# Performance work log

Hardware: AMD Instinct MI355X
Metric: run time of the kernel (lower is better)

## Reference

```python
import jax, jax.numpy as jnp
import numpy as np

EPS = 1e-10
COMMITMENT_COST = 0.25


def setup_inputs() -> dict:
    key = jax.random.key(0)
    k1, k2, k3, k4 = jax.random.split(key, 4)
    return {
        "x": jax.random.normal(k1, (32, 64, 64, 64), dtype=jnp.float32),  # NCHW, C=D=64
        "emb0": jax.random.normal(k2, (512, 64), dtype=jnp.float32),
        "emb1": jax.random.normal(k3, (512, 64), dtype=jnp.float32),
        "emb2": jax.random.normal(k4, (512, 64), dtype=jnp.float32),
        "idx": 1,
    }


def reference(x, emb0, emb1, emb2, idx):
    # NCHW -> NHWC, flatten to [N, D]
    inputs = jnp.transpose(x, (0, 2, 3, 1))
    in_shape = inputs.shape
    D = in_shape[-1]
    flat = inputs.reshape(-1, D)  # [N, D]

    if idx == 0:
        codes = emb0
    elif idx == 1:
        codes = jnp.concatenate([emb0, emb1], axis=0)
    else:
        codes = jnp.concatenate([emb0, emb2], axis=0)  # [K, D]

    distances = (
        jnp.sum(flat * flat, axis=1, keepdims=True)
        + jnp.sum(codes * codes, axis=1)
        - 2.0 * jnp.matmul(flat, codes.T)
    )
    enc_idx = jnp.argmin(distances, axis=1)  # [N]

    # one-hot @ codes is just a gather
    quantized = codes[enc_idx].reshape(in_shape)

    e_latent_loss = jnp.mean((jax.lax.stop_gradient(quantized) - inputs) ** 2)
    q_latent_loss = jnp.mean((quantized - jax.lax.stop_gradient(inputs)) ** 2)
    loss = q_latent_loss + COMMITMENT_COST * e_latent_loss

    # straight-through estimator
    quantized_st = inputs + jax.lax.stop_gradient(quantized - inputs)

    K = codes.shape[0]
    N = flat.shape[0]
    avg_probs = jnp.zeros((K,), dtype=flat.dtype).at[enc_idx].add(1.0) / N
    perplexity = jnp.exp(-jnp.sum(avg_probs * jnp.log(avg_probs + EPS)))

    return jnp.transpose(quantized_st, (0, 3, 1, 2)), loss, perplexity
```

## Files before the change

### kernel.cpp

```cpp
#include <hip/hip_runtime.h>
#include <math.h>

#define NROWS   131072
#define DFEAT   64
#define KHALF   512
#define HW      4096
#define CHW     262144
#define NQOUT   8388608

typedef __attribute__((ext_vector_type(8))) short   bf16x8;
typedef __attribute__((ext_vector_type(4))) float   f32x4;

__device__ __forceinline__ unsigned short f2bf(float f) {
    unsigned int u = __float_as_uint(f);
    u += 0x7FFFu + ((u >> 16) & 1u);
    return (unsigned short)(u >> 16);
}
__device__ __forceinline__ float bf2f(unsigned short h) {
    return __uint_as_float(((unsigned int)h) << 16);
}

__global__ void vq_cnorm(const float* __restrict__ e0, const float* __restrict__ e1,
                         const float* __restrict__ e2, const int* __restrict__ idxp,
                         float* __restrict__ cnh) {
    int k = blockIdx.x * blockDim.x + threadIdx.x;
    if (k >= 1024) return;
    int idx = idxp[0];
    const float* sel = (idx == 2) ? e2 : e1;
    const float* row = (k < KHALF) ? (e0 + (size_t)k * DFEAT)
                                   : (sel + (size_t)(k - KHALF) * DFEAT);
    float s = 0.f;
#pragma unroll
    for (int c = 0; c < DFEAT; ++c) s = fmaf(row[c], row[c], s);
    cnh[k] = 0.5f * s;
}

__global__ void vq_pack(const float* __restrict__ e0, const float* __restrict__ e1,
                        const float* __restrict__ e2, const int* __restrict__ idxp,
                        unsigned short* __restrict__ fragbuf) {
    int tau = blockIdx.x * 256 + threadIdx.x;
    int tile = tau >> 8;
    int rem  = tau & 255;
    int f    = rem >> 6;
    int L    = rem & 63;
    int code = tile * 16 + (L & 15);
    int kb   = (f & 1) * 32 + (L >> 4) * 8;
    int lo_f = f >> 1;
    int idx  = idxp[0];
    const float* sel = (idx == 2) ? e2 : e1;
    const float* src = (code < KHALF) ? (e0 + (size_t)code * DFEAT)
                                      : (sel + (size_t)(code - KHALF) * DFEAT);
    unsigned short* dst = fragbuf + (size_t)tau * 8;
#pragma unroll
    for (int j = 0; j < 8; ++j) {
        float v = src[kb + j];
        unsigned short hb = f2bf(v);
        dst[j] = lo_f ? f2bf(v - bf2f(hb)) : hb;
    }
}

__global__ __launch_bounds__(256, 2) void vq_main(
        const float* __restrict__ x,
        const float* __restrict__ e0, const float* __restrict__ e1,
        const float* __restrict__ e2, const int* __restrict__ idxp,
        const float* __restrict__ cnh, const unsigned short* __restrict__ fragbuf,
        float* __restrict__ out, float* __restrict__ loss_acc,
        int* __restrict__ hist) {
    __shared__ float xsq_s[256];
    __shared__ float sc_s[256];
    __shared__ int   bk_s[256];

    const int t = threadIdx.x;
    const int w = t >> 6;
    const int L = t & 63;
    const int q = L >> 4;
    const int m = L & 15;

    const int rowbase = blockIdx.x * 256;
    const int n  = rowbase >> 12;
    const int s0 = rowbase & 4095;

    const int idx = idxp[0];
    const float* sel = (idx == 2) ? e2 : e1;
    const int ntiles = (idx == 0) ? 32 : 64;

    bf16x8 ahi[4][2], alo[4][2];
    const float* xb = x + (size_t)n * CHW + (s0 + w * 64);
#pragma unroll
    for (int rt = 0; rt < 4; ++rt) {
        const float* xr = xb + rt * 16 + m;
        float xs = 0.f;
#pragma unroll
        for (int h = 0; h < 2; ++h) {
#pragma unroll
            for (int j = 0; j < 8; ++j) {
                int c = h * 32 + q * 8 + j;
                float v = xr[(size_t)c * HW];
                xs = fmaf(v, v, xs);
                unsigned short hb = f2bf(v);
                unsigned short lb = f2bf(v - bf2f(hb));
                ahi[rt][h][j] = (short)hb;
                alo[rt][h][j] = (short)lb;
            }
        }
        xs += __shfl_xor(xs, 16, 64);
        xs += __shfl_xor(xs, 32, 64);
        if (q == 0) xsq_s[w * 64 + rt * 16 + m] = xs;
    }

    const bf16x8* fb = (const bf16x8*)fragbuf;
    float best[16];
    int   bidx[16];
#pragma unroll
    for (int i = 0; i < 16; ++i) { best[i] = -3.4e38f; bidx[i] = 0; }

    bf16x8 bc0 = fb[0 * 64 + L];
    bf16x8 bc1 = fb[1 * 64 + L];
    bf16x8 bc2 = fb[2 * 64 + L];
    bf16x8 bc3 = fb[3 * 64 + L];
    float  cnc = cnh[m];

    for (int tt = 0; tt < ntiles; ++tt) {
        const int tn = (tt + 1 < ntiles) ? tt + 1 : tt;
        bf16x8 bn0 = fb[(tn * 4 + 0) * 64 + L];
        bf16x8 bn1 = fb[(tn * 4 + 1) * 64 + L];
        bf16x8 bn2 = fb[(tn * 4 + 2) * 64 + L];
        bf16x8 bn3 = fb[(tn * 4 + 3) * 64 + L];
        float  cnn = cnh[tn * 16 + m];
        const int kt = tt * 16 + m;
#pragma unroll
        for (int rt = 0; rt < 4; ++rt) {
            f32x4 acc = {0.f, 0.f, 0.f, 0.f};
            acc = __builtin_amdgcn_mfma_f32_16x16x32_bf16(ahi[rt][0], bc0, acc, 0, 0, 0);
            acc = __builtin_amdgcn_mfma_f32_16x16x32_bf16(ahi[rt][1], bc1, acc, 0, 0, 0);
            acc = __builtin_amdgcn_mfma_f32_16x16x32_bf16(ahi[rt][0], bc2, acc, 0, 0, 0);
            acc = __builtin_amdgcn_mfma_f32_16x16x32_bf16(ahi[rt][1], bc3, acc, 0, 0, 0);
            acc = __builtin_amdgcn_mfma_f32_16x16x32_bf16(alo[rt][0], bc0, acc, 0, 0, 0);
            acc = __builtin_amdgcn_mfma_f32_16x16x32_bf16(alo[rt][1], bc1, acc, 0, 0, 0);
            acc = __builtin_amdgcn_mfma_f32_16x16x32_bf16(alo[rt][0], bc2, acc, 0, 0, 0);
            acc = __builtin_amdgcn_mfma_f32_16x16x32_bf16(alo[rt][1], bc3, acc, 0, 0, 0);
#pragma unroll
            for (int r = 0; r < 4; ++r) {
                float s = acc[r] - cnc;
                if (s > best[rt * 4 + r]) { best[rt * 4 + r] = s; bidx[rt * 4 + r] = kt; }
            }
        }
        bc0 = bn0; bc1 = bn1; bc2 = bn2; bc3 = bn3; cnc = cnn;
    }

#pragma unroll
    for (int i = 0; i < 16; ++i) {
        float b = best[i]; int k = bidx[i];
#pragma unroll
        for (int off = 1; off < 16; off <<= 1) {
            float ob = __shfl_xor(b, off, 64);
            int   ok = __shfl_xor(k, off, 64);
            if (ob > b || (ob == b && ok < k)) { b = ob; k = ok; }
        }
        if (m == 0) {
            int row = w * 64 + (i >> 2) * 16 + q * 4 + (i & 3);
            sc_s[row] = b; bk_s[row] = k;
        }
    }
    __syncthreads();

    const int k   = bk_s[t];
    float dist    = xsq_s[t] - 2.f * sc_s[t];
    float l = dist;
#pragma unroll
    for (int off = 32; off > 0; off >>= 1) l += __shfl_down(l, off, 64);
    if (L == 0) atomicAdd(loss_acc, l);
    atomicAdd(&hist[k], 1);

    const float* cp = (k < KHALF) ? (e0 + (size_t)k * DFEAT)
                                  : (sel + (size_t)(k - KHALF) * DFEAT);
    const float4* cp4 = (const float4*)cp;
    float* op = out + (size_t)n * CHW + (s0 + t);
#pragma unroll
    for (int c4 = 0; c4 < 16; ++c4) {
        float4 v = cp4[c4];
        op[(size_t)(4 * c4 + 0) * HW] = v.x;
        op[(size_t)(4 * c4 + 1) * HW] = v.y;
        op[(size_t)(4 * c4 + 2) * HW] = v.z;
        op[(size_t)(4 * c4 + 3) * HW] = v.w;
    }
}

__global__ void vq_finalize(const float* __restrict__ wsf, const int* __restrict__ hist,
                            float* __restrict__ out) {
    __shared__ double partial[16];
    const int t = threadIdx.x;
    double p = (double)hist[t] / (double)NROWS;
    double term = p * log(p + 1e-10);
#pragma unroll
    for (int off = 32; off > 0; off >>= 1) term += __shfl_down(term, off, 64);
    if ((t & 63) == 0) partial[t >> 6] = term;
    __syncthreads();
    if (t == 0) {
        double s = 0.0;
        for (int i = 0; i < 16; ++i) s += partial[i];
        out[NQOUT + 1] = (float)exp(-s);
        out[NQOUT]     = 1.25f * (wsf[0] / (float)NQOUT);
    }
}

extern "C" void kernel_launch(void* const* d_in, const int* in_sizes, int n_in,
                              void* d_out, int out_size, void* d_ws, size_t ws_size,
                              hipStream_t stream) {
    const float* x  = (const float*)d_in[0];
    const float* e0 = (const float*)d_in[1];
    const float* e1 = (const float*)d_in[2];
    const float* e2 = (const float*)d_in[3];
    const int* idxp = (const int*)d_in[4];
    float* out = (float*)d_out;

    float* wsf      = (float*)d_ws;
    float* loss_acc = wsf;
    int*   hist     = (int*)(wsf + 256);
    float* cnh      = wsf + 2048;
    unsigned short* fragbuf = (unsigned short*)(wsf + 4096);

    hipMemsetAsync(d_ws, 0, 1280 * sizeof(float), stream);
    vq_cnorm<<<4, 256, 0, stream>>>(e0, e1, e2, idxp, cnh);
    vq_pack<<<64, 256, 0, stream>>>(e0, e1, e2, idxp, fragbuf);
    vq_main<<<NROWS / 256, 256, 0, stream>>>(x, e0, e1, e2, idxp, cnh, fragbuf,
                                             out, loss_acc, hist);
    vq_finalize<<<1, 1024, 0, stream>>>(wsf, hist, out);
}
```

Before: 193.8 us.

## Fuse prep kernels, halve rows per block, and finalize in last block

Merges the memset, codebook-norm and fragment-pack kernels into one prep kernel, and folds the perplexity/loss finalize into the main kernel using a last-block-done atomic counter. Each main block now handles 128 rows instead of 256, which doubles the grid to 1024 blocks, raises the launch-bounds occupancy target to 4, and splits the output scatter across all 256 threads. The aim is to cut launch overhead and improve latency hiding. The trade-off is that each codebook fragment load is reused over fewer rows, so fragment traffic per row doubles, and the threadfence plus completion counter add some serialization.

```diff
diff --git a/kernel.cpp b/kernel.cpp
--- a/kernel.cpp
+++ b/kernel.cpp
@@ -7,6 +7,7 @@
 #define HW      4096
 #define CHW     262144
 #define NQOUT   8388608
+#define NBLK    1024
 
 typedef __attribute__((ext_vector_type(8))) short   bf16x8;
 typedef __attribute__((ext_vector_type(4))) float   f32x4;
@@ -20,25 +21,25 @@
     return __uint_as_float(((unsigned int)h) << 16);
 }
 
-__global__ void vq_cnorm(const float* __restrict__ e0, const float* __restrict__ e1,
-                         const float* __restrict__ e2, const int* __restrict__ idxp,
-                         float* __restrict__ cnh) {
-    int k = blockIdx.x * blockDim.x + threadIdx.x;
-    if (k >= 1024) return;
+__global__ void vq_prep(const float* __restrict__ e0, const float* __restrict__ e1,
+                        const float* __restrict__ e2, const int* __restrict__ idxp,
+                        float* __restrict__ wsf, float* __restrict__ cnh,
+                        unsigned short* __restrict__ fragbuf) {
+    int tau = blockIdx.x * 256 + threadIdx.x;
+    if (tau < 1536) wsf[tau] = 0.f;
+
     int idx = idxp[0];
     const float* sel = (idx == 2) ? e2 : e1;
-    const float* row = (k < KHALF) ? (e0 + (size_t)k * DFEAT)
-                                   : (sel + (size_t)(k - KHALF) * DFEAT);
-    float s = 0.f;
-#pragma unroll
-    for (int c = 0; c < DFEAT; ++c) s = fmaf(row[c], row[c], s);
-    cnh[k] = 0.5f * s;
-}
-
-__global__ void vq_pack(const float* __restrict__ e0, const float* __restrict__ e1,
-                        const float* __restrict__ e2, const int* __restrict__ idxp,
-                        unsigned short* __restrict__ fragbuf) {
-    int tau = blockIdx.x * 256 + threadIdx.x;
+
+    if (tau < 1024) {
+        const float* row = (tau < KHALF) ? (e0 + (size_t)tau * DFEAT)
+                                         : (sel + (size_t)(tau - KHALF) * DFEAT);
+        float s = 0.f;
+#pragma unroll
+        for (int c = 0; c < DFEAT; ++c) s = fmaf(row[c], row[c], s);
+        cnh[tau] = 0.5f * s;
+    }
+
     int tile = tau >> 8;
     int rem  = tau & 255;
     int f    = rem >> 6;
@@ -46,8 +47,6 @@
     int code = tile * 16 + (L & 15);
     int kb   = (f & 1) * 32 + (L >> 4) * 8;
     int lo_f = f >> 1;
-    int idx  = idxp[0];
-    const float* sel = (idx == 2) ? e2 : e1;
     const float* src = (code < KHALF) ? (e0 + (size_t)code * DFEAT)
                                       : (sel + (size_t)(code - KHALF) * DFEAT);
     unsigned short* dst = fragbuf + (size_t)tau * 8;
@@ -59,16 +58,18 @@
     }
 }
 
-__global__ __launch_bounds__(256, 2) void vq_main(
+__global__ __launch_bounds__(256, 4) void vq_main(
         const float* __restrict__ x,
         const float* __restrict__ e0, const float* __restrict__ e1,
         const float* __restrict__ e2, const int* __restrict__ idxp,
         const float* __restrict__ cnh, const unsigned short* __restrict__ fragbuf,
         float* __restrict__ out, float* __restrict__ loss_acc,
-        int* __restrict__ hist) {
-    __shared__ float xsq_s[256];
-    __shared__ float sc_s[256];
-    __shared__ int   bk_s[256];
+        int* __restrict__ hist, int* __restrict__ done_ctr) {
+    __shared__ float  xsq_s[128];
+    __shared__ float  sc_s[128];
+    __shared__ int    bk_s[128];
+    __shared__ int    islast_s;
+    __shared__ double pp_s[4];
 
     const int t = threadIdx.x;
     const int w = t >> 6;
@@ -76,7 +77,7 @@
     const int q = L >> 4;
     const int m = L & 15;
 
-    const int rowbase = blockIdx.x * 256;
+    const int rowbase = blockIdx.x * 128;
     const int n  = rowbase >> 12;
     const int s0 = rowbase & 4095;
 
@@ -84,10 +85,10 @@
     const float* sel = (idx == 2) ? e2 : e1;
     const int ntiles = (idx == 0) ? 32 : 64;
 
-    bf16x8 ahi[4][2], alo[4][2];
-    const float* xb = x + (size_t)n * CHW + (s0 + w * 64);
-#pragma unroll
-    for (int rt = 0; rt < 4; ++rt) {
+    bf16x8 ahi[2][2], alo[2][2];
+    const float* xb = x + (size_t)n * CHW + (s0 + w * 32);
+#pragma unroll
+    for (int rt = 0; rt < 2; ++rt) {
         const float* xr = xb + rt * 16 + m;
         float xs = 0.f;
 #pragma unroll
@@ -105,14 +106,14 @@
         }
         xs += __shfl_xor(xs, 16, 64);
         xs += __shfl_xor(xs, 32, 64);
-        if (q == 0) xsq_s[w * 64 + rt * 16 + m] = xs;
+        if (q == 0) xsq_s[w * 32 + rt * 16 + m] = xs;
     }
 
     const bf16x8* fb = (const bf16x8*)fragbuf;
-    float best[16];
-    int   bidx[16];
-#pragma unroll
-    for (int i = 0; i < 16; ++i) { best[i] = -3.4e38f; bidx[i] = 0; }
+    float best[8];
+    int   bidx[8];
+#pragma unroll
+    for (int i = 0; i < 8; ++i) { best[i] = -3.4e38f; bidx[i] = 0; }
 
     bf16x8 bc0 = fb[0 * 64 + L];
     bf16x8 bc1 = fb[1 * 64 + L];
@@ -120,6 +121,7 @@
     bf16x8 bc3 = fb[3 * 64 + L];
     float  cnc = cnh[m];
 
+#pragma unroll 2
     for (int tt = 0; tt < ntiles; ++tt) {
         const int tn = (tt + 1 < ntiles) ? tt + 1 : tt;
         bf16x8 bn0 = fb[(tn * 4 + 0) * 64 + L];
@@ -129,7 +131,7 @@
         float  cnn = cnh[tn * 16 + m];
         const int kt = tt * 16 + m;
 #pragma unroll
-        for (int rt = 0; rt < 4; ++rt) {
+        for (int rt = 0; rt < 2; ++rt) {
             f32x4 acc = {0.f, 0.f, 0.f, 0.f};
             acc = __builtin_amdgcn_mfma_f32_16x16x32_bf16(ahi[rt][0], bc0, acc, 0, 0, 0);
             acc = __builtin_amdgcn_mfma_f32_16x16x32_bf16(ahi[rt][1], bc1, acc, 0, 0, 0);
@@ -149,7 +151,7 @@
     }
 
 #pragma unroll
-    for (int i = 0; i < 16; ++i) {
+    for (int i = 0; i < 8; ++i) {
         float b = best[i]; int k = bidx[i];
 #pragma unroll
         for (int off = 1; off < 16; off <<= 1) {
@@ -158,49 +160,69 @@
             if (ob > b || (ob == b && ok < k)) { b = ob; k = ok; }
         }
         if (m == 0) {
-            int row = w * 64 + (i >> 2) * 16 + q * 4 + (i & 3);
+            int row = w * 32 + (i >> 2) * 16 + q * 4 + (i & 3);
             sc_s[row] = b; bk_s[row] = k;
         }
     }
     __syncthreads();
 
-    const int k   = bk_s[t];
-    float dist    = xsq_s[t] - 2.f * sc_s[t];
-    float l = dist;
-#pragma unroll
-    for (int off = 32; off > 0; off >>= 1) l += __shfl_down(l, off, 64);
-    if (L == 0) atomicAdd(loss_acc, l);
-    atomicAdd(&hist[k], 1);
-
-    const float* cp = (k < KHALF) ? (e0 + (size_t)k * DFEAT)
-                                  : (sel + (size_t)(k - KHALF) * DFEAT);
-    const float4* cp4 = (const float4*)cp;
-    float* op = out + (size_t)n * CHW + (s0 + t);
-#pragma unroll
-    for (int c4 = 0; c4 < 16; ++c4) {
-        float4 v = cp4[c4];
-        op[(size_t)(4 * c4 + 0) * HW] = v.x;
-        op[(size_t)(4 * c4 + 1) * HW] = v.y;
-        op[(size_t)(4 * c4 + 2) * HW] = v.z;
-        op[(size_t)(4 * c4 + 3) * HW] = v.w;
-    }
-}
-
-__global__ void vq_finalize(const float* __restrict__ wsf, const int* __restrict__ hist,
-                            float* __restrict__ out) {
-    __shared__ double partial[16];
-    const int t = threadIdx.x;
-    double p = (double)hist[t] / (double)NROWS;
-    double term = p * log(p + 1e-10);
-#pragma unroll
-    for (int off = 32; off > 0; off >>= 1) term += __shfl_down(term, off, 64);
-    if ((t & 63) == 0) partial[t >> 6] = term;
+    if (t < 128) {
+        const int k = bk_s[t];
+        float dist = xsq_s[t] - 2.f * sc_s[t];
+        float l = dist;
+#pragma unroll
+        for (int off = 32; off > 0; off >>= 1) l += __shfl_down(l, off, 64);
+        if (L == 0) atomicAdd(loss_acc, l);
+        atomicAdd(&hist[k], 1);
+    }
+
+    {
+        const int row  = t & 127;
+        const int half = t >> 7;
+        const int k = bk_s[row];
+        const float* cp = ((k < KHALF) ? (e0 + (size_t)k * DFEAT)
+                                       : (sel + (size_t)(k - KHALF) * DFEAT)) + half * 32;
+        const float4* cp4 = (const float4*)cp;
+        float* op = out + (size_t)n * CHW + (s0 + row);
+#pragma unroll
+        for (int c4 = 0; c4 < 8; ++c4) {
+            float4 v = cp4[c4];
+            int c = half * 32 + 4 * c4;
+            op[(size_t)(c + 0) * HW] = v.x;
+            op[(size_t)(c + 1) * HW] = v.y;
+            op[(size_t)(c + 2) * HW] = v.z;
+            op[(size_t)(c + 3) * HW] = v.w;
+        }
+    }
+
+    __threadfence();
     __syncthreads();
     if (t == 0) {
-        double s = 0.0;
-        for (int i = 0; i < 16; ++i) s += partial[i];
-        out[NQOUT + 1] = (float)exp(-s);
-        out[NQOUT]     = 1.25f * (wsf[0] / (float)NQOUT);
+        int tk = __hip_atomic_fetch_add(done_ctr, 1, __ATOMIC_ACQ_REL,
+                                        __HIP_MEMORY_SCOPE_AGENT);
+        islast_s = (tk == NBLK - 1);
+    }
+    __syncthreads();
+    if (islast_s) {
+        double term = 0.0;
+#pragma unroll
+        for (int j = 0; j < 4; ++j) {
+            int c = __hip_atomic_load(&hist[t * 4 + j], __ATOMIC_RELAXED,
+                                      __HIP_MEMORY_SCOPE_AGENT);
+            double p = (double)c / (double)NROWS;
+            term += p * log(p + 1e-10);
+        }
+#pragma unroll
+        for (int off = 32; off > 0; off >>= 1) term += __shfl_down(term, off, 64);
+        if (L == 0) pp_s[w] = term;
+        __syncthreads();
+        if (t == 0) {
+            double s = pp_s[0] + pp_s[1] + pp_s[2] + pp_s[3];
+            float lacc = __hip_atomic_load(loss_acc, __ATOMIC_RELAXED,
+                                           __HIP_MEMORY_SCOPE_AGENT);
+            out[NQOUT + 1] = (float)exp(-s);
+            out[NQOUT]     = 1.25f * (lacc / (float)NQOUT);
+        }
     }
 }
 
@@ -217,13 +239,11 @@
     float* wsf      = (float*)d_ws;
     float* loss_acc = wsf;
     int*   hist     = (int*)(wsf + 256);
+    int*   done_ctr = (int*)(wsf + 1280);
     float* cnh      = wsf + 2048;
     unsigned short* fragbuf = (unsigned short*)(wsf + 4096);
 
-    hipMemsetAsync(d_ws, 0, 1280 * sizeof(float), stream);
-    vq_cnorm<<<4, 256, 0, stream>>>(e0, e1, e2, idxp, cnh);
-    vq_pack<<<64, 256, 0, stream>>>(e0, e1, e2, idxp, fragbuf);
-    vq_main<<<NROWS / 256, 256, 0, stream>>>(x, e0, e1, e2, idxp, cnh, fragbuf,
-                                             out, loss_acc, hist);
-    vq_finalize<<<1, 1024, 0, stream>>>(wsf, hist, out);
-}
+    vq_prep<<<64, 256, 0, stream>>>(e0, e1, e2, idxp, wsf, cnh, fragbuf);
+    vq_main<<<NBLK, 256, 0, stream>>>(x, e0, e1, e2, idxp, cnh, fragbuf,
+                                      out, loss_acc, hist, done_ctr);
+}
```

New measurement: 292.0 us. 50.7% more time.
